# Kernel tuning notes

Measured on AMD Instinct MI355X. Metric: run time of the kernel, lower is better.

## Reference

```python
import jax, jax.numpy as jnp
import numpy as np
from math import sqrt

B, L, S, H, E = 4, 2048, 2048, 16, 64


def setup_inputs() -> dict:
    key = jax.random.key(0)
    kq, kk, kv = jax.random.split(key, 3)
    queries = jax.random.normal(kq, (B, L, H, E), dtype=jnp.float32)
    keys = jax.random.normal(kk, (B, S, H, E), dtype=jnp.float32)
    values = jax.random.normal(kv, (B, S, H, E), dtype=jnp.float32)
    # causal mask: True where attention is disallowed (upper triangle, excl diag)
    causal = jnp.triu(jnp.ones((L, S), dtype=jnp.bool_), k=1)
    attention_mask = jnp.broadcast_to(causal[None, None, :, :], (B, 1, L, S))
    return {"queries": queries, "keys": keys, "values": values,
            "attention_mask": attention_mask}


def reference(queries, keys, values, attention_mask):
    E_ = queries.shape[-1]
    scale = 1.0 / sqrt(E_)
    # [B,H,L,S] full score matrix (the quadratic intermediate of naive attention)
    scores = jnp.einsum('blhe,bshe->bhls', queries, keys)
    scores = jnp.where(attention_mask, -jnp.inf, scores)
    A = jnp.nan_to_num(jax.nn.softmax(scale * scores, axis=-1))
    V = jnp.einsum('bhls,bshd->blhd', A, values)
    return V
```

## Files before the change

kernel.cpp:

```cpp
#include <hip/hip_runtime.h>
#include <cmath>
#include <type_traits>

#define B_ 4
#define L_ 2048
#define S_ 2048
#define H_ 16
#define E_ 64
#define SCALE2 0.18033688011112042f

typedef __attribute__((ext_vector_type(4))) float f32x4;
typedef __attribute__((ext_vector_type(8))) __bf16 bf16x8;
typedef __attribute__((ext_vector_type(8))) unsigned short ushort8;
union FragU { ushort8 u; bf16x8 b; unsigned int d[4]; };

__device__ __forceinline__ unsigned short f2bf(float f) {
    unsigned int u = __float_as_uint(f);
    return (unsigned short)((u + 0x7FFFu + ((u >> 16) & 1u)) >> 16);
}

__device__ __forceinline__ unsigned int pack_bf(float hi, float lo) {
    return __builtin_amdgcn_perm(__float_as_uint(hi), __float_as_uint(lo),
                                 0x07060302u);
}

__device__ __forceinline__ void gload_lds16(const void* g, void* l) {
    __builtin_amdgcn_global_load_lds(
        (const __attribute__((address_space(1))) void*)g,
        (__attribute__((address_space(3))) void*)l, 16, 0, 0);
}

__global__ __launch_bounds__(256) void conv_k(const float* __restrict__ K,
                                              unsigned short* __restrict__ Kbf) {
    const int idx = blockIdx.x * 256 + threadIdx.x;
    const int j   = idx & 7;
    const int row = idx >> 3;
    const int s   = row & (S_ - 1);
    const int bh  = row >> 11;
    const int h   = bh & (H_ - 1);
    const int b   = bh >> 4;
    const int jp  = j ^ (s & 7);
    const float* src = K + (((size_t)b * S_ + s) * H_ + h) * E_ + jp * 8;
    f32x4 a = *(const f32x4*)src;
    f32x4 d = *(const f32x4*)(src + 4);
    ushort8 u;
    u[0]=f2bf(a[0]); u[1]=f2bf(a[1]); u[2]=f2bf(a[2]); u[3]=f2bf(a[3]);
    u[4]=f2bf(d[0]); u[5]=f2bf(d[1]); u[6]=f2bf(d[2]); u[7]=f2bf(d[3]);
    *(ushort8*)(Kbf + (size_t)row * E_ + j * 8) = u;
}

__global__ __launch_bounds__(256) void conv_v(const float* __restrict__ V,
                                              unsigned short* __restrict__ Vt) {
    __shared__ unsigned short t[64 * 65];
    const int tid  = threadIdx.x;
    const int sblk = blockIdx.x & 31;
    const int h    = (blockIdx.x >> 5) & 15;
    const int b    = blockIdx.x >> 9;
    const int s0   = sblk * 64;
    for (int i = 0; i < 4; ++i) {
        const int c = tid + i * 256;
        const int sr = c >> 4, e0 = (c & 15) * 4;
        f32x4 a = *(const f32x4*)(V + (((size_t)b * S_ + s0 + sr) * H_ + h) * E_ + e0);
        t[sr * 65 + e0 + 0] = f2bf(a[0]);
        t[sr * 65 + e0 + 1] = f2bf(a[1]);
        t[sr * 65 + e0 + 2] = f2bf(a[2]);
        t[sr * 65 + e0 + 3] = f2bf(a[3]);
    }
    __syncthreads();
    for (int i = 0; i < 2; ++i) {
        const int c  = tid + i * 256;
        const int e  = c >> 3, cc = c & 7;
        const int q  = cc >> 1, half = cc & 1;
        ushort8 u;
        for (int j = 0; j < 8; ++j) {
            const int d = j >> 2, r = j & 3;
            const int key = (2 * half + d) * 16 + q * 4 + r;
            u[j] = t[key * 65 + e];
        }
        *(ushort8*)(Vt + ((size_t)(b * H_ + h) * E_ + e) * S_ + s0
                    + (cc ^ (e & 7)) * 8) = u;
    }
}

template <bool PRE>
__global__ __launch_bounds__(256, 4) void fattn_kernel(
    const float* __restrict__ Q, const unsigned short* __restrict__ Kbf,
    const unsigned short* __restrict__ Vt, const float* __restrict__ Kf,
    const float* __restrict__ Vf, float* __restrict__ Out)
{
    const int tid  = threadIdx.x;
    const int wave = tid >> 6;
    const int lane = tid & 63;
    const int ln   = lane & 15;
    const int quad = lane >> 4;
    const int h = blockIdx.x;
    const int b = blockIdx.z;
    const int qtile = (blockIdx.y + blockIdx.x + 4 * blockIdx.z) & 15;
    const int q0 = qtile * 128;
    const int qw = q0 + wave * 32;
    const int p7 = ln & 7;

    __shared__ __align__(16) unsigned short ldsK[2][64 * 64];
    __shared__ __align__(16) unsigned short ldsV[2][64 * 64];

    FragU qf[2][2];
    #pragma unroll
    for (int g = 0; g < 2; ++g) {
        const float* qp = Q + (((size_t)b * L_ + (qw + g * 16 + ln)) * H_ + h) * E_;
        #pragma unroll
        for (int c = 0; c < 2; ++c) {
            const int e0 = c * 32 + quad * 8;
            f32x4 lo = *(const f32x4*)(qp + e0);
            f32x4 hi = *(const f32x4*)(qp + e0 + 4);
            ushort8 u;
            u[0]=f2bf(lo[0]*SCALE2); u[1]=f2bf(lo[1]*SCALE2);
            u[2]=f2bf(lo[2]*SCALE2); u[3]=f2bf(lo[3]*SCALE2);
            u[4]=f2bf(hi[0]*SCALE2); u[5]=f2bf(hi[1]*SCALE2);
            u[6]=f2bf(hi[2]*SCALE2); u[7]=f2bf(hi[3]*SCALE2);
            qf[g][c].u = u;
        }
    }

    FragU onef;
    #pragma unroll
    for (int j = 0; j < 8; ++j) onef.u[j] = 0x3F80;

    f32x4 o[2][4];
    #pragma unroll
    for (int g = 0; g < 2; ++g)
        #pragma unroll
        for (int et = 0; et < 4; ++et) o[g][et] = f32x4{0.f, 0.f, 0.f, 0.f};
    f32x4 lacc[2];
    lacc[0] = f32x4{0.f, 0.f, 0.f, 0.f};
    lacc[1] = f32x4{0.f, 0.f, 0.f, 0.f};

    const unsigned short* kbh = Kbf + (size_t)(b * H_ + h) * S_ * E_;
    const unsigned short* vbh = Vt  + (size_t)(b * H_ + h) * E_ * S_;
    const float* kf32 = Kf + (((size_t)b * S_) * H_ + h) * E_;
    const float* vf32 = Vf + (((size_t)b * S_) * H_ + h) * E_;

    auto STAGE = [&](int bsel, int kt2) {
        const int k0s = kt2 * 64;
        if constexpr (PRE) {
            const unsigned short* ktb = kbh + (size_t)k0s * E_;
            const unsigned short* vtb = vbh + k0s;
            #pragma unroll
            for (int i = 0; i < 2; ++i) {
                const int slot0 = wave * 128 + i * 64;
                gload_lds16(ktb + (size_t)(slot0 + lane) * 8,
                            &ldsK[bsel][slot0 * 8]);
            }
            #pragma unroll
            for (int i = 0; i < 2; ++i) {
                const int slot0 = wave * 128 + i * 64;
                const int slot  = slot0 + lane;
                const int e = slot >> 3, lc = slot & 7;
                gload_lds16(vtb + (size_t)e * S_ + lc * 8,
                            &ldsV[bsel][slot0 * 8]);
            }
        } else {
            #pragma unroll
            for (int i = 0; i < 2; ++i) {
                const int c = tid + i * 256;
                const int key = c >> 3, j = c & 7, jp = j ^ (key & 7);
                const float* src = kf32 + (size_t)(k0s + key) * (H_ * E_) + jp * 8;
                f32x4 a = *(const f32x4*)src, d = *(const f32x4*)(src + 4);
                ushort8 u;
                u[0]=f2bf(a[0]); u[1]=f2bf(a[1]); u[2]=f2bf(a[2]); u[3]=f2bf(a[3]);
                u[4]=f2bf(d[0]); u[5]=f2bf(d[1]); u[6]=f2bf(d[2]); u[7]=f2bf(d[3]);
                *(ushort8*)&ldsK[bsel][key * 64 + j * 8] = u;
            }
            #pragma unroll
            for (int i = 0; i < 2; ++i) {
                const int c = tid + i * 256;
                const int e = c >> 3, cc = c & 7;
                const int q = cc >> 1, half = cc & 1;
                ushort8 u;
                #pragma unroll
                for (int j = 0; j < 8; ++j) {
                    const int d = j >> 2, r = j & 3;
                    const int key = (2 * half + d) * 16 + q * 4 + r;
                    u[j] = f2bf(vf32[(size_t)(k0s + key) * (H_ * E_) + e]);
                }
                *(ushort8*)&ldsV[bsel][e * 64 + (cc ^ (e & 7)) * 8] = u;
            }
        }
    };

    const int ntiles = 2 * qtile + 2;
    STAGE(0, 0);
    int cur = 0;
    for (int kt = 0; kt < ntiles; ++kt) {
        const int k0 = kt * 64;
        __syncthreads();
        if (kt + 1 < ntiles) STAGE(cur ^ 1, kt + 1);

        if (k0 <= qw + 31) {
            __builtin_amdgcn_s_setprio(1);
            const unsigned short* bK = ldsK[cur];
            const unsigned short* bV = ldsV[cur];
            FragU pf[2][2];

            auto qk_phase = [&](auto masked) {
                #pragma unroll
                for (int n = 0; n < 4; ++n) {
                    FragU kf0, kf1;
                    kf0.u = *(const ushort8*)&bK[(n*16+ln)*64 + ((quad    ) ^ p7) * 8];
                    kf1.u = *(const ushort8*)&bK[(n*16+ln)*64 + ((4 + quad) ^ p7) * 8];
                    #pragma unroll
                    for (int g = 0; g < 2; ++g) {
                        f32x4 acc = f32x4{0.f, 0.f, 0.f, 0.f};
                        acc = __builtin_amdgcn_mfma_f32_16x16x32_bf16(kf0.b, qf[g][0].b, acc, 0, 0, 0);
                        acc = __builtin_amdgcn_mfma_f32_16x16x32_bf16(kf1.b, qf[g][1].b, acc, 0, 0, 0);
                        float p[4];
                        #pragma unroll
                        for (int r = 0; r < 4; ++r) {
                            float v = __builtin_exp2f(acc[r]);
                            if constexpr (decltype(masked)::value) {
                                const int key  = k0 + n * 16 + quad * 4 + r;
                                const int qrow = qw + g * 16 + ln;
                                v = (key <= qrow) ? v : 0.f;
                            }
                            p[r] = v;
                        }
                        pf[g][n >> 1].d[(n & 1) * 2 + 0] = pack_bf(p[1], p[0]);
                        pf[g][n >> 1].d[(n & 1) * 2 + 1] = pack_bf(p[3], p[2]);
                    }
                }
            };
            if (k0 + 63 > qw) qk_phase(std::integral_constant<bool, true>{});
            else              qk_phase(std::integral_constant<bool, false>{});

            #pragma unroll
            for (int g = 0; g < 2; ++g) {
                lacc[g] = __builtin_amdgcn_mfma_f32_16x16x32_bf16(pf[g][0].b, onef.b, lacc[g], 0, 0, 0);
                lacc[g] = __builtin_amdgcn_mfma_f32_16x16x32_bf16(pf[g][1].b, onef.b, lacc[g], 0, 0, 0);
            }
            #pragma unroll
            for (int et = 0; et < 4; ++et) {
                FragU vf0, vf1;
                vf0.u = *(const ushort8*)&bV[(et*16+ln)*64 + ((2*quad    ) ^ p7) * 8];
                vf1.u = *(const ushort8*)&bV[(et*16+ln)*64 + ((2*quad + 1) ^ p7) * 8];
                #pragma unroll
                for (int g = 0; g < 2; ++g) {
                    o[g][et] = __builtin_amdgcn_mfma_f32_16x16x32_bf16(pf[g][0].b, vf0.b, o[g][et], 0, 0, 0);
                    o[g][et] = __builtin_amdgcn_mfma_f32_16x16x32_bf16(pf[g][1].b, vf1.b, o[g][et], 0, 0, 0);
                }
            }
            __builtin_amdgcn_s_setprio(0);
        }
        cur ^= 1;
    }

    #pragma unroll
    for (int g = 0; g < 2; ++g) {
        #pragma unroll
        for (int r = 0; r < 4; ++r) {
            const float invr = 1.f / lacc[g][r];
            float* op = Out + (((size_t)b * L_ + (qw + g * 16 + quad * 4 + r)) * H_ + h) * E_;
            #pragma unroll
            for (int et = 0; et < 4; ++et)
                op[et * 16 + ln] = o[g][et][r] * invr;
        }
    }
}

extern "C" void kernel_launch(void* const* d_in, const int* in_sizes, int n_in,
                              void* d_out, int out_size, void* d_ws, size_t ws_size,
                              hipStream_t stream) {
    const float* Q = (const float*)d_in[0];
    const float* K = (const float*)d_in[1];
    const float* V = (const float*)d_in[2];
    float* Out = (float*)d_out;

    const size_t plane = (size_t)B_ * H_ * S_ * E_;
    unsigned short* Kbf = (unsigned short*)d_ws;
    unsigned short* Vt  = Kbf + plane;

    dim3 grid(H_, L_ / 128, B_);
    if (ws_size >= plane * 2 * sizeof(unsigned short)) {
        conv_k<<<(int)(plane / 8 / 256), 256, 0, stream>>>(K, Kbf);
        conv_v<<<B_ * H_ * (S_ / 64), 256, 0, stream>>>(V, Vt);
        fattn_kernel<true><<<grid, dim3(256), 0, stream>>>(Q, Kbf, Vt, K, V, Out);
    } else {
        fattn_kernel<false><<<grid, dim3(256), 0, stream>>>(Q, Kbf, Vt, K, V, Out);
    }
}
```

Before: 228.4 us.

## Split K/V staging into triple-buffered K and double-buffered V pipeline with explicit waitcnts

```diff
diff --git a/kernel.cpp b/kernel.cpp
--- a/kernel.cpp
+++ b/kernel.cpp
@@ -95,12 +95,13 @@
     const int quad = lane >> 4;
     const int h = blockIdx.x;
     const int b = blockIdx.z;
-    const int qtile = (blockIdx.y + blockIdx.x + 4 * blockIdx.z) & 15;
+    const int tt = (blockIdx.y + ((blockIdx.z >> 1) << 3)) & 15;
+    const int qtile = (blockIdx.z & 1) ? (15 - tt) : tt;
     const int q0 = qtile * 128;
     const int qw = q0 + wave * 32;
     const int p7 = ln & 7;
 
-    __shared__ __align__(16) unsigned short ldsK[2][64 * 64];
+    __shared__ __align__(16) unsigned short ldsK[3][64 * 64];
     __shared__ __align__(16) unsigned short ldsV[2][64 * 64];
 
     FragU qf[2][2];
@@ -139,24 +140,15 @@
     const float* kf32 = Kf + (((size_t)b * S_) * H_ + h) * E_;
     const float* vf32 = Vf + (((size_t)b * S_) * H_ + h) * E_;
 
-    auto STAGE = [&](int bsel, int kt2) {
+    auto STAGE_K = [&](int bsel, int kt2) {
         const int k0s = kt2 * 64;
         if constexpr (PRE) {
             const unsigned short* ktb = kbh + (size_t)k0s * E_;
-            const unsigned short* vtb = vbh + k0s;
             #pragma unroll
             for (int i = 0; i < 2; ++i) {
                 const int slot0 = wave * 128 + i * 64;
                 gload_lds16(ktb + (size_t)(slot0 + lane) * 8,
                             &ldsK[bsel][slot0 * 8]);
-            }
-            #pragma unroll
-            for (int i = 0; i < 2; ++i) {
-                const int slot0 = wave * 128 + i * 64;
-                const int slot  = slot0 + lane;
-                const int e = slot >> 3, lc = slot & 7;
-                gload_lds16(vtb + (size_t)e * S_ + lc * 8,
-                            &ldsV[bsel][slot0 * 8]);
             }
         } else {
             #pragma unroll
@@ -170,6 +162,21 @@
                 u[4]=f2bf(d[0]); u[5]=f2bf(d[1]); u[6]=f2bf(d[2]); u[7]=f2bf(d[3]);
                 *(ushort8*)&ldsK[bsel][key * 64 + j * 8] = u;
             }
+        }
+    };
+    auto STAGE_V = [&](int bsel, int kt2) {
+        const int k0s = kt2 * 64;
+        if constexpr (PRE) {
+            const unsigned short* vtb = vbh + k0s;
+            #pragma unroll
+            for (int i = 0; i < 2; ++i) {
+                const int slot0 = wave * 128 + i * 64;
+                const int slot  = slot0 + lane;
+                const int e = slot >> 3, lc = slot & 7;
+                gload_lds16(vtb + (size_t)e * S_ + lc * 8,
+                            &ldsV[bsel][slot0 * 8]);
+            }
+        } else {
             #pragma unroll
             for (int i = 0; i < 2; ++i) {
                 const int c = tid + i * 256;
@@ -188,19 +195,33 @@
     };
 
     const int ntiles = 2 * qtile + 2;
-    STAGE(0, 0);
-    int cur = 0;
+    STAGE_K(0, 0);
+    STAGE_V(0, 0);
+    STAGE_K(1, 1);
+
+    int kb = 0;
     for (int kt = 0; kt < ntiles; ++kt) {
         const int k0 = kt * 64;
-        __syncthreads();
-        if (kt + 1 < ntiles) STAGE(cur ^ 1, kt + 1);
-
-        if (k0 <= qw + 31) {
+        const bool active = (k0 <= qw + 31);
+
+        if (kt + 1 < ntiles)
+            asm volatile("s_waitcnt vmcnt(4) lgkmcnt(0)" ::: "memory");
+        else
+            asm volatile("s_waitcnt vmcnt(0) lgkmcnt(0)" ::: "memory");
+        __builtin_amdgcn_s_barrier();
+        __builtin_amdgcn_sched_barrier(0);
+
+        if (kt + 1 < ntiles) STAGE_V((kt + 1) & 1, kt + 1);
+        if (kt + 2 < ntiles) {
+            int kb2 = kb + 2; if (kb2 >= 3) kb2 -= 3;
+            STAGE_K(kb2, kt + 2);
+        }
+        __builtin_amdgcn_sched_barrier(0);
+
+        FragU pf[2][2];
+        if (active) {
             __builtin_amdgcn_s_setprio(1);
-            const unsigned short* bK = ldsK[cur];
-            const unsigned short* bV = ldsV[cur];
-            FragU pf[2][2];
-
+            const unsigned short* bK = ldsK[kb];
             auto qk_phase = [&](auto masked) {
                 #pragma unroll
                 for (int n = 0; n < 4; ++n) {
@@ -230,7 +251,19 @@
             };
             if (k0 + 63 > qw) qk_phase(std::integral_constant<bool, true>{});
             else              qk_phase(std::integral_constant<bool, false>{});
-
+            __builtin_amdgcn_s_setprio(0);
+        }
+
+        if (kt + 2 < ntiles)
+            asm volatile("s_waitcnt vmcnt(6) lgkmcnt(0)" ::: "memory");
+        else
+            asm volatile("s_waitcnt vmcnt(0) lgkmcnt(0)" ::: "memory");
+        __builtin_amdgcn_s_barrier();
+        __builtin_amdgcn_sched_barrier(0);
+
+        if (active) {
+            __builtin_amdgcn_s_setprio(1);
+            const unsigned short* bV = ldsV[kt & 1];
             #pragma unroll
             for (int g = 0; g < 2; ++g) {
                 lacc[g] = __builtin_amdgcn_mfma_f32_16x16x32_bf16(pf[g][0].b, onef.b, lacc[g], 0, 0, 0);
@@ -249,7 +282,7 @@
             }
             __builtin_amdgcn_s_setprio(0);
         }
-        cur ^= 1;
+        ++kb; if (kb == 3) kb = 0;
     }
 
     #pragma unroll
```

After: 229.5 us. No clear change (+0.5%).

## Drop LDS staging and load K/V fragments straight from global per wave

Applied to the files above, without the earlier changes.

```diff
diff --git a/kernel.cpp b/kernel.cpp
--- a/kernel.cpp
+++ b/kernel.cpp
@@ -22,12 +22,6 @@
 __device__ __forceinline__ unsigned int pack_bf(float hi, float lo) {
     return __builtin_amdgcn_perm(__float_as_uint(hi), __float_as_uint(lo),
                                  0x07060302u);
-}
-
-__device__ __forceinline__ void gload_lds16(const void* g, void* l) {
-    __builtin_amdgcn_global_load_lds(
-        (const __attribute__((address_space(1))) void*)g,
-        (__attribute__((address_space(3))) void*)l, 16, 0, 0);
 }
 
 __global__ __launch_bounds__(256) void conv_k(const float* __restrict__ K,
@@ -95,13 +89,11 @@
     const int quad = lane >> 4;
     const int h = blockIdx.x;
     const int b = blockIdx.z;
-    const int qtile = (blockIdx.y + blockIdx.x + 4 * blockIdx.z) & 15;
+    const int tt = (blockIdx.y + ((blockIdx.z >> 1) << 3)) & 15;
+    const int qtile = (blockIdx.z & 1) ? (15 - tt) : tt;
     const int q0 = qtile * 128;
     const int qw = q0 + wave * 32;
     const int p7 = ln & 7;
-
-    __shared__ __align__(16) unsigned short ldsK[2][64 * 64];
-    __shared__ __align__(16) unsigned short ldsV[2][64 * 64];
 
     FragU qf[2][2];
     #pragma unroll
@@ -139,118 +131,101 @@
     const float* kf32 = Kf + (((size_t)b * S_) * H_ + h) * E_;
     const float* vf32 = Vf + (((size_t)b * S_) * H_ + h) * E_;
 
-    auto STAGE = [&](int bsel, int kt2) {
-        const int k0s = kt2 * 64;
+    const int ntw = ((qw + 31) >> 6) + 1;
+
+    auto tile = [&](int kt, auto masked) {
+        const int k0 = kt * 64;
+        FragU kf[8];
         if constexpr (PRE) {
-            const unsigned short* ktb = kbh + (size_t)k0s * E_;
-            const unsigned short* vtb = vbh + k0s;
-            #pragma unroll
-            for (int i = 0; i < 2; ++i) {
-                const int slot0 = wave * 128 + i * 64;
-                gload_lds16(ktb + (size_t)(slot0 + lane) * 8,
-                            &ldsK[bsel][slot0 * 8]);
-            }
-            #pragma unroll
-            for (int i = 0; i < 2; ++i) {
-                const int slot0 = wave * 128 + i * 64;
-                const int slot  = slot0 + lane;
-                const int e = slot >> 3, lc = slot & 7;
-                gload_lds16(vtb + (size_t)e * S_ + lc * 8,
-                            &ldsV[bsel][slot0 * 8]);
+            #pragma unroll
+            for (int n = 0; n < 4; ++n) {
+                const unsigned short* kr = kbh + (size_t)(k0 + n * 16 + ln) * E_;
+                kf[2*n  ].u = *(const ushort8*)(kr + ((quad    ) ^ p7) * 8);
+                kf[2*n+1].u = *(const ushort8*)(kr + ((4 + quad) ^ p7) * 8);
             }
         } else {
             #pragma unroll
-            for (int i = 0; i < 2; ++i) {
-                const int c = tid + i * 256;
-                const int key = c >> 3, j = c & 7, jp = j ^ (key & 7);
-                const float* src = kf32 + (size_t)(k0s + key) * (H_ * E_) + jp * 8;
-                f32x4 a = *(const f32x4*)src, d = *(const f32x4*)(src + 4);
-                ushort8 u;
-                u[0]=f2bf(a[0]); u[1]=f2bf(a[1]); u[2]=f2bf(a[2]); u[3]=f2bf(a[3]);
-                u[4]=f2bf(d[0]); u[5]=f2bf(d[1]); u[6]=f2bf(d[2]); u[7]=f2bf(d[3]);
-                *(ushort8*)&ldsK[bsel][key * 64 + j * 8] = u;
-            }
-            #pragma unroll
-            for (int i = 0; i < 2; ++i) {
-                const int c = tid + i * 256;
-                const int e = c >> 3, cc = c & 7;
-                const int q = cc >> 1, half = cc & 1;
-                ushort8 u;
+            for (int n = 0; n < 4; ++n) {
+                const float* kr = kf32 + (size_t)(k0 + n * 16 + ln) * (H_ * E_);
                 #pragma unroll
-                for (int j = 0; j < 8; ++j) {
-                    const int d = j >> 2, r = j & 3;
-                    const int key = (2 * half + d) * 16 + q * 4 + r;
-                    u[j] = f2bf(vf32[(size_t)(k0s + key) * (H_ * E_) + e]);
+                for (int c = 0; c < 2; ++c) {
+                    f32x4 a = *(const f32x4*)(kr + (c * 4 + quad) * 8);
+                    f32x4 d = *(const f32x4*)(kr + (c * 4 + quad) * 8 + 4);
+                    ushort8 u;
+                    u[0]=f2bf(a[0]); u[1]=f2bf(a[1]); u[2]=f2bf(a[2]); u[3]=f2bf(a[3]);
+                    u[4]=f2bf(d[0]); u[5]=f2bf(d[1]); u[6]=f2bf(d[2]); u[7]=f2bf(d[3]);
+                    kf[2*n+c].u = u;
                 }
-                *(ushort8*)&ldsV[bsel][e * 64 + (cc ^ (e & 7)) * 8] = u;
-            }
-        }
+            }
+        }
+        FragU vf[8];
+        if constexpr (PRE) {
+            #pragma unroll
+            for (int et = 0; et < 4; ++et) {
+                const unsigned short* vr = vbh + (size_t)(et * 16 + ln) * S_ + k0;
+                vf[2*et  ].u = *(const ushort8*)(vr + ((2 * quad    ) ^ p7) * 8);
+                vf[2*et+1].u = *(const ushort8*)(vr + ((2 * quad + 1) ^ p7) * 8);
+            }
+        } else {
+            #pragma unroll
+            for (int et = 0; et < 4; ++et) {
+                const int e = et * 16 + ln;
+                #pragma unroll
+                for (int half = 0; half < 2; ++half) {
+                    ushort8 u;
+                    #pragma unroll
+                    for (int j = 0; j < 8; ++j) {
+                        const int key = half * 32 + (j >> 2) * 16 + quad * 4 + (j & 3);
+                        u[j] = f2bf(vf32[(size_t)(k0 + key) * (H_ * E_) + e]);
+                    }
+                    vf[2*et+half].u = u;
+                }
+            }
+        }
+
+        FragU pf[2][2];
+        __builtin_amdgcn_s_setprio(1);
+        #pragma unroll
+        for (int n = 0; n < 4; ++n) {
+            #pragma unroll
+            for (int g = 0; g < 2; ++g) {
+                f32x4 acc = f32x4{0.f, 0.f, 0.f, 0.f};
+                acc = __builtin_amdgcn_mfma_f32_16x16x32_bf16(kf[2*n].b,   qf[g][0].b, acc, 0, 0, 0);
+                acc = __builtin_amdgcn_mfma_f32_16x16x32_bf16(kf[2*n+1].b, qf[g][1].b, acc, 0, 0, 0);
+                float p[4];
+                #pragma unroll
+                for (int r = 0; r < 4; ++r) {
+                    float v = __builtin_exp2f(acc[r]);
+                    if constexpr (decltype(masked)::value) {
+                        const int key  = k0 + n * 16 + quad * 4 + r;
+                        const int qrow = qw + g * 16 + ln;
+                        v = (key <= qrow) ? v : 0.f;
+                    }
+                    p[r] = v;
+                }
+                pf[g][n >> 1].d[(n & 1) * 2 + 0] = pack_bf(p[1], p[0]);
+                pf[g][n >> 1].d[(n & 1) * 2 + 1] = pack_bf(p[3], p[2]);
+            }
+        }
+        #pragma unroll
+        for (int g = 0; g < 2; ++g) {
+            lacc[g] = __builtin_amdgcn_mfma_f32_16x16x32_bf16(pf[g][0].b, onef.b, lacc[g], 0, 0, 0);
+            lacc[g] = __builtin_amdgcn_mfma_f32_16x16x32_bf16(pf[g][1].b, onef.b, lacc[g], 0, 0, 0);
+        }
+        #pragma unroll
+        for (int et = 0; et < 4; ++et) {
+            #pragma unroll
+            for (int g = 0; g < 2; ++g) {
+                o[g][et] = __builtin_amdgcn_mfma_f32_16x16x32_bf16(pf[g][0].b, vf[2*et].b,   o[g][et], 0, 0, 0);
+                o[g][et] = __builtin_amdgcn_mfma_f32_16x16x32_bf16(pf[g][1].b, vf[2*et+1].b, o[g][et], 0, 0, 0);
+            }
+        }
+        __builtin_amdgcn_s_setprio(0);
     };
 
-    const int ntiles = 2 * qtile + 2;
-    STAGE(0, 0);
-    int cur = 0;
-    for (int kt = 0; kt < ntiles; ++kt) {
-        const int k0 = kt * 64;
-        __syncthreads();
-        if (kt + 1 < ntiles) STAGE(cur ^ 1, kt + 1);
-
-        if (k0 <= qw + 31) {
-            __builtin_amdgcn_s_setprio(1);
-            const unsigned short* bK = ldsK[cur];
-            const unsigned short* bV = ldsV[cur];
-            FragU pf[2][2];
-
-            auto qk_phase = [&](auto masked) {
-                #pragma unroll
-                for (int n = 0; n < 4; ++n) {
-                    FragU kf0, kf1;
-                    kf0.u = *(const ushort8*)&bK[(n*16+ln)*64 + ((quad    ) ^ p7) * 8];
-                    kf1.u = *(const ushort8*)&bK[(n*16+ln)*64 + ((4 + quad) ^ p7) * 8];
-                    #pragma unroll
-                    for (int g = 0; g < 2; ++g) {
-                        f32x4 acc = f32x4{0.f, 0.f, 0.f, 0.f};
-                        acc = __builtin_amdgcn_mfma_f32_16x16x32_bf16(kf0.b, qf[g][0].b, acc, 0, 0, 0);
-                        acc = __builtin_amdgcn_mfma_f32_16x16x32_bf16(kf1.b, qf[g][1].b, acc, 0, 0, 0);
-                        float p[4];
-                        #pragma unroll
-                        for (int r = 0; r < 4; ++r) {
-                            float v = __builtin_exp2f(acc[r]);
-                            if constexpr (decltype(masked)::value) {
-                                const int key  = k0 + n * 16 + quad * 4 + r;
-                                const int qrow = qw + g * 16 + ln;
-                                v = (key <= qrow) ? v : 0.f;
-                            }
-                            p[r] = v;
-                        }
-                        pf[g][n >> 1].d[(n & 1) * 2 + 0] = pack_bf(p[1], p[0]);
-                        pf[g][n >> 1].d[(n & 1) * 2 + 1] = pack_bf(p[3], p[2]);
-                    }
-                }
-            };
-            if (k0 + 63 > qw) qk_phase(std::integral_constant<bool, true>{});
-            else              qk_phase(std::integral_constant<bool, false>{});
-
-            #pragma unroll
-            for (int g = 0; g < 2; ++g) {
-                lacc[g] = __builtin_amdgcn_mfma_f32_16x16x32_bf16(pf[g][0].b, onef.b, lacc[g], 0, 0, 0);
-                lacc[g] = __builtin_amdgcn_mfma_f32_16x16x32_bf16(pf[g][1].b, onef.b, lacc[g], 0, 0, 0);
-            }
-            #pragma unroll
-            for (int et = 0; et < 4; ++et) {
-                FragU vf0, vf1;
-                vf0.u = *(const ushort8*)&bV[(et*16+ln)*64 + ((2*quad    ) ^ p7) * 8];
-                vf1.u = *(const ushort8*)&bV[(et*16+ln)*64 + ((2*quad + 1) ^ p7) * 8];
-                #pragma unroll
-                for (int g = 0; g < 2; ++g) {
-                    o[g][et] = __builtin_amdgcn_mfma_f32_16x16x32_bf16(pf[g][0].b, vf0.b, o[g][et], 0, 0, 0);
-                    o[g][et] = __builtin_amdgcn_mfma_f32_16x16x32_bf16(pf[g][1].b, vf1.b, o[g][et], 0, 0, 0);
-                }
-            }
-            __builtin_amdgcn_s_setprio(0);
-        }
-        cur ^= 1;
-    }
+    for (int kt = 0; kt + 1 < ntw; ++kt)
+        tile(kt, std::integral_constant<bool, false>{});
+    tile(ntw - 1, std::integral_constant<bool, true>{});
 
     #pragma unroll
     for (int g = 0; g < 2; ++g) {
```

After: 317.0 us. 38.8% more time.

## Load V fragments directly from global in MFMA-native layout, drop V LDS staging

Applied to the files above, without the earlier changes.

```diff
diff --git a/kernel.cpp b/kernel.cpp
--- a/kernel.cpp
+++ b/kernel.cpp
@@ -68,17 +68,18 @@
     }
     __syncthreads();
     for (int i = 0; i < 2; ++i) {
-        const int c  = tid + i * 256;
-        const int e  = c >> 3, cc = c & 7;
-        const int q  = cc >> 1, half = cc & 1;
+        const int m  = tid + i * 256;
+        const int et = m >> 7;
+        const int c  = (m >> 6) & 1;
+        const int qd = (m >> 4) & 3;
+        const int l2 = m & 15;
         ushort8 u;
         for (int j = 0; j < 8; ++j) {
-            const int d = j >> 2, r = j & 3;
-            const int key = (2 * half + d) * 16 + q * 4 + r;
-            u[j] = t[key * 65 + e];
-        }
-        *(ushort8*)(Vt + ((size_t)(b * H_ + h) * E_ + e) * S_ + s0
-                    + (cc ^ (e & 7)) * 8) = u;
+            const int kk = (2 * c + (j >> 2)) * 16 + qd * 4 + (j & 3);
+            u[j] = t[kk * 65 + et * 16 + l2];
+        }
+        *(ushort8*)(Vt + (size_t)(b * H_ + h) * (S_ * E_)
+                    + (size_t)sblk * 4096 + (size_t)m * 8) = u;
     }
 }
 
@@ -95,13 +96,13 @@
     const int quad = lane >> 4;
     const int h = blockIdx.x;
     const int b = blockIdx.z;
-    const int qtile = (blockIdx.y + blockIdx.x + 4 * blockIdx.z) & 15;
+    const int tt = (blockIdx.y + ((blockIdx.z >> 1) << 3)) & 15;
+    const int qtile = (blockIdx.z & 1) ? (15 - tt) : tt;
     const int q0 = qtile * 128;
     const int qw = q0 + wave * 32;
     const int p7 = ln & 7;
 
     __shared__ __align__(16) unsigned short ldsK[2][64 * 64];
-    __shared__ __align__(16) unsigned short ldsV[2][64 * 64];
 
     FragU qf[2][2];
     #pragma unroll
@@ -135,28 +136,19 @@
     lacc[1] = f32x4{0.f, 0.f, 0.f, 0.f};
 
     const unsigned short* kbh = Kbf + (size_t)(b * H_ + h) * S_ * E_;
-    const unsigned short* vbh = Vt  + (size_t)(b * H_ + h) * E_ * S_;
+    const unsigned short* vbh = Vt  + (size_t)(b * H_ + h) * (S_ * E_);
     const float* kf32 = Kf + (((size_t)b * S_) * H_ + h) * E_;
     const float* vf32 = Vf + (((size_t)b * S_) * H_ + h) * E_;
 
-    auto STAGE = [&](int bsel, int kt2) {
+    auto STAGE_K = [&](int bsel, int kt2) {
         const int k0s = kt2 * 64;
         if constexpr (PRE) {
             const unsigned short* ktb = kbh + (size_t)k0s * E_;
-            const unsigned short* vtb = vbh + k0s;
             #pragma unroll
             for (int i = 0; i < 2; ++i) {
                 const int slot0 = wave * 128 + i * 64;
                 gload_lds16(ktb + (size_t)(slot0 + lane) * 8,
                             &ldsK[bsel][slot0 * 8]);
-            }
-            #pragma unroll
-            for (int i = 0; i < 2; ++i) {
-                const int slot0 = wave * 128 + i * 64;
-                const int slot  = slot0 + lane;
-                const int e = slot >> 3, lc = slot & 7;
-                gload_lds16(vtb + (size_t)e * S_ + lc * 8,
-                            &ldsV[bsel][slot0 * 8]);
             }
         } else {
             #pragma unroll
@@ -170,37 +162,44 @@
                 u[4]=f2bf(d[0]); u[5]=f2bf(d[1]); u[6]=f2bf(d[2]); u[7]=f2bf(d[3]);
                 *(ushort8*)&ldsK[bsel][key * 64 + j * 8] = u;
             }
-            #pragma unroll
-            for (int i = 0; i < 2; ++i) {
-                const int c = tid + i * 256;
-                const int e = c >> 3, cc = c & 7;
-                const int q = cc >> 1, half = cc & 1;
-                ushort8 u;
-                #pragma unroll
-                for (int j = 0; j < 8; ++j) {
-                    const int d = j >> 2, r = j & 3;
-                    const int key = (2 * half + d) * 16 + q * 4 + r;
-                    u[j] = f2bf(vf32[(size_t)(k0s + key) * (H_ * E_) + e]);
-                }
-                *(ushort8*)&ldsV[bsel][e * 64 + (cc ^ (e & 7)) * 8] = u;
-            }
         }
     };
 
+    auto vload_f32 = [&](int k0s, int et, int c, FragU& dst) {
+        ushort8 u;
+        #pragma unroll
+        for (int j = 0; j < 8; ++j) {
+            const int key = k0s + (2 * c + (j >> 2)) * 16 + quad * 4 + (j & 3);
+            u[j] = f2bf(vf32[(size_t)key * (H_ * E_) + et * 16 + ln]);
+        }
+        dst.u = u;
+    };
+
     const int ntiles = 2 * qtile + 2;
-    STAGE(0, 0);
+    STAGE_K(0, 0);
     int cur = 0;
     for (int kt = 0; kt < ntiles; ++kt) {
         const int k0 = kt * 64;
         __syncthreads();
-        if (kt + 1 < ntiles) STAGE(cur ^ 1, kt + 1);
+        if (kt + 1 < ntiles) STAGE_K(cur ^ 1, kt + 1);
 
         if (k0 <= qw + 31) {
+            const unsigned short* bK  = ldsK[cur];
+            const unsigned short* vtb = vbh + (size_t)kt * 4096;
+
+            FragU vc0, vc1, vn0, vn1;
+            if constexpr (PRE) {
+                vc0.u = *(const ushort8*)(vtb + 0 * 512 + lane * 8);
+                vc1.u = *(const ushort8*)(vtb + 1 * 512 + lane * 8);
+                vn0.u = *(const ushort8*)(vtb + 2 * 512 + lane * 8);
+                vn1.u = *(const ushort8*)(vtb + 3 * 512 + lane * 8);
+            } else {
+                vload_f32(k0, 0, 0, vc0); vload_f32(k0, 0, 1, vc1);
+                vload_f32(k0, 1, 0, vn0); vload_f32(k0, 1, 1, vn1);
+            }
+
             __builtin_amdgcn_s_setprio(1);
-            const unsigned short* bK = ldsK[cur];
-            const unsigned short* bV = ldsV[cur];
             FragU pf[2][2];
-
             auto qk_phase = [&](auto masked) {
                 #pragma unroll
                 for (int n = 0; n < 4; ++n) {
@@ -238,13 +237,21 @@
             }
             #pragma unroll
             for (int et = 0; et < 4; ++et) {
-                FragU vf0, vf1;
-                vf0.u = *(const ushort8*)&bV[(et*16+ln)*64 + ((2*quad    ) ^ p7) * 8];
-                vf1.u = *(const ushort8*)&bV[(et*16+ln)*64 + ((2*quad + 1) ^ p7) * 8];
+                FragU va = vc0, vb = vc1;
+                vc0 = vn0; vc1 = vn1;
+                if (et < 2) {
+                    if constexpr (PRE) {
+                        vn0.u = *(const ushort8*)(vtb + (2*(et+2)    ) * 512 + lane * 8);
+                        vn1.u = *(const ushort8*)(vtb + (2*(et+2) + 1) * 512 + lane * 8);
+                    } else {
+                        vload_f32(k0, et + 2, 0, vn0);
+                        vload_f32(k0, et + 2, 1, vn1);
+                    }
+                }
                 #pragma unroll
                 for (int g = 0; g < 2; ++g) {
-                    o[g][et] = __builtin_amdgcn_mfma_f32_16x16x32_bf16(pf[g][0].b, vf0.b, o[g][et], 0, 0, 0);
-                    o[g][et] = __builtin_amdgcn_mfma_f32_16x16x32_bf16(pf[g][1].b, vf1.b, o[g][et], 0, 0, 0);
+                    o[g][et] = __builtin_amdgcn_mfma_f32_16x16x32_bf16(pf[g][0].b, va.b, o[g][et], 0, 0, 0);
+                    o[g][et] = __builtin_amdgcn_mfma_f32_16x16x32_bf16(pf[g][1].b, vb.b, o[g][et], 0, 0, 0);
                 }
             }
             __builtin_amdgcn_s_setprio(0);
```

Result: no change. 228.2 us (-0.1%).
